# Kernel tuning notes

Hardware: AMD Instinct MI355X
Metric: run time of the kernel (lower is better)

## Reference

```python
import jax, jax.numpy as jnp
import numpy as np

N = 100000      # nodes
E = 1600000     # edges (avg degree 16)
D_IN = 128
CONV_SIZES = [64, 64]
FC_SIZES = [64, 32, 1]


def _glorot(key, shape):
    lim = np.sqrt(6.0 / (shape[0] + shape[1]))
    return jax.random.uniform(key, shape, jnp.float32, -lim, lim)


def setup_inputs() -> dict:
    key = jax.random.key(0)
    ks = jax.random.split(key, 2 + len(CONV_SIZES) + len(FC_SIZES))
    inp = {
        "x": jax.random.normal(ks[0], (N, D_IN), jnp.float32),
        "edge_index": jax.random.randint(ks[1], (2, E), 0, N, dtype=jnp.int64),
    }
    size = D_IN
    ki = 2
    for li, s in enumerate(CONV_SIZES):
        inp[f"cW{li}"] = _glorot(ks[ki], (size, s)); ki += 1
        inp[f"cb{li}"] = jnp.zeros((s,), jnp.float32)
        size = s
    for li, s in enumerate(FC_SIZES):
        inp[f"fW{li}"] = _glorot(ks[ki], (size, s)); ki += 1
        inp[f"fb{li}"] = jnp.zeros((s,), jnp.float32)
        size = s
    return inp


def gcn_conv(x, src, dst, W, b, n_nodes):
    """PyG GCNConv: symmetric normalization with added self-loops."""
    xl = x @ W  # [N, out]
    # degree including self-loop
    deg = jnp.zeros((n_nodes,), xl.dtype).at[dst].add(1.0) + 1.0
    dinv = jax.lax.rsqrt(deg)
    norm = dinv[src] * dinv[dst]                 # [E]
    msg = xl[src] * norm[:, None]                # gather + scale, [E, out]
    agg = jax.ops.segment_sum(msg, dst, num_segments=n_nodes)
    # self-loop contribution: norm = 1/deg
    return agg + xl * (1.0 / deg)[:, None] + b


def reference(x, edge_index, cW0, cb0, cW1, cb1, fW0, fb0, fW1, fb1, fW2, fb2):
    src, dst = edge_index[0], edge_index[1]
    h = jnp.tanh(gcn_conv(x, src, dst, cW0, cb0, N))
    h = jnp.tanh(gcn_conv(h, src, dst, cW1, cb1, N))
    h = jnp.tanh(h @ fW0 + fb0)
    h = jnp.tanh(h @ fW1 + fb1)
    return h @ fW2 + fb2  # [N, 1]
```

## Files before the change

### kernel.cpp

```cpp
#include <hip/hip_runtime.h>
#include <math.h>

#define N_NODES 100000
#define N_EDGES 1600000
#define NB     391
#define CHUNK  4096
#define NBLK_A 391

typedef unsigned short ushort_t;

__device__ inline unsigned short f2bf(float f) {
    unsigned u = __float_as_uint(f);
    unsigned r = (u + 0x7FFFu + ((u >> 16) & 1u)) >> 16;
    return (unsigned short)r;
}
__device__ inline void acc2(float& a0, float& a1, unsigned u) {
    a0 += __uint_as_float(u << 16);
    a1 += __uint_as_float(u & 0xFFFF0000u);
}


__global__ __launch_bounds__(256) void k_count(const int* __restrict__ dst,
                                               unsigned* __restrict__ cnt) {
    __shared__ unsigned h[NB];
    const int tid = threadIdx.x;
    const long e0 = (long)blockIdx.x * CHUNK;
    for (int i = tid; i < NB; i += 256) h[i] = 0u;
    __syncthreads();
    for (int i = tid; i < CHUNK; i += 256) {
        long e = e0 + i;
        if (e < N_EDGES) atomicAdd(&h[((unsigned)dst[e]) >> 8], 1u);
    }
    __syncthreads();
    for (int b = tid; b < NB; b += 256) cnt[b * NBLK_A + blockIdx.x] = h[b];
}

__global__ __launch_bounds__(512) void k_bucket_scan(unsigned* __restrict__ cnt,
                                                     unsigned* __restrict__ btot) {
    __shared__ unsigned s[512];
    const int tid = threadIdx.x;
    const int b = blockIdx.x;
    unsigned v = (tid < NBLK_A) ? cnt[b * NBLK_A + tid] : 0u;
    s[tid] = v;
    __syncthreads();
    for (int o = 1; o < 512; o <<= 1) {
        unsigned t = (tid >= o) ? s[tid - o] : 0u;
        __syncthreads();
        s[tid] += t;
        __syncthreads();
    }
    if (tid < NBLK_A) cnt[b * NBLK_A + tid] = s[tid] - v;
    if (tid == NBLK_A - 1) btot[b] = s[tid];
}

__global__ __launch_bounds__(512) void k_scan_bkt(const unsigned* __restrict__ btot,
                                                  unsigned* __restrict__ bktbase) {
    __shared__ unsigned s[512];
    const int tid = threadIdx.x;
    unsigned v = (tid < NB) ? btot[tid] : 0u;
    s[tid] = v;
    __syncthreads();
    for (int o = 1; o < 512; o <<= 1) {
        unsigned t = (tid >= o) ? s[tid - o] : 0u;
        __syncthreads();
        s[tid] += t;
        __syncthreads();
    }
    if (tid < NB) bktbase[tid] = s[tid] - v;
    if (tid == NB - 1) bktbase[NB] = s[tid];
}

__global__ __launch_bounds__(256) void k_bin(const int* __restrict__ src,
                                             const int* __restrict__ dst,
                                             const unsigned* __restrict__ cnt,
                                             const unsigned* __restrict__ bktbase,
                                             unsigned* __restrict__ binned) {
    __shared__ unsigned cntA[NB];
    __shared__ unsigned excl[NB];
    __shared__ unsigned gbase[NB];
    __shared__ unsigned scanbuf[512];
    __shared__ unsigned data[CHUNK];
    const int tid = threadIdx.x;
    const long e0 = (long)blockIdx.x * CHUNK;

    for (int i = tid; i < NB; i += 256) cntA[i] = 0u;
    __syncthreads();
    for (int i = tid; i < CHUNK; i += 256) {
        long e = e0 + i;
        if (e < N_EDGES) atomicAdd(&cntA[((unsigned)dst[e]) >> 8], 1u);
    }
    __syncthreads();
    scanbuf[tid] = (tid < NB) ? cntA[tid] : 0u;
    scanbuf[tid + 256] = (tid + 256 < NB) ? cntA[tid + 256] : 0u;
    __syncthreads();
    for (int o = 1; o < 512; o <<= 1) {
        unsigned v0 = (tid >= o) ? scanbuf[tid - o] : 0u;
        unsigned v1 = (tid + 256 >= o) ? scanbuf[tid + 256 - o] : 0u;
        __syncthreads();
        scanbuf[tid] += v0;
        scanbuf[tid + 256] += v1;
        __syncthreads();
    }
    for (int b = tid; b < NB; b += 256) {
        excl[b] = scanbuf[b] - cntA[b];
        gbase[b] = bktbase[b] + cnt[b * NBLK_A + blockIdx.x];
    }
    __syncthreads();
    for (int i = tid; i < NB; i += 256) cntA[i] = 0u;
    __syncthreads();
    for (int i = tid; i < CHUNK; i += 256) {
        long e = e0 + i;
        if (e < N_EDGES) {
            unsigned d = (unsigned)dst[e];
            unsigned b = d >> 8;
            unsigned slot = excl[b] + atomicAdd(&cntA[b], 1u);
            data[slot] = (((unsigned)src[e]) << 8) | (d & 255u);
        }
    }
    __syncthreads();
    const int w = tid >> 6, lane = tid & 63;
    for (int b = w; b < NB; b += 4) {
        unsigned c = cntA[b];
        unsigned sb = excl[b], gb = gbase[b];
        for (unsigned k = lane; k < c; k += 64)
            binned[gb + k] = data[sb + k];
    }
}

__global__ __launch_bounds__(256) void k_csr_fill2(const unsigned* __restrict__ binned,
                                                   const unsigned* __restrict__ bktbase,
                                                   unsigned* __restrict__ rowptr,
                                                   float* __restrict__ dinv,
                                                   int* __restrict__ ssrc) {
    __shared__ unsigned cnt[256];
    __shared__ unsigned s[256];
    __shared__ unsigned cur[256];
    const int b = blockIdx.x;
    const int tid = threadIdx.x;
    const int n0 = b * 256;
    const unsigned beg = bktbase[b], end = bktbase[b + 1];
    cnt[tid] = 0u;
    __syncthreads();
    for (unsigned i = beg + tid; i < end; i += 256)
        atomicAdd(&cnt[binned[i] & 255u], 1u);
    __syncthreads();
    const unsigned v = cnt[tid];
    s[tid] = v;
    __syncthreads();
    for (int o = 1; o < 256; o <<= 1) {
        unsigned t = (tid >= o) ? s[tid - o] : 0u;
        __syncthreads();
        s[tid] += t;
        __syncthreads();
    }
    const unsigned excl = s[tid] - v;
    const int node = n0 + tid;
    if (node < N_NODES) {
        rowptr[node] = beg + excl;
        dinv[node] = rsqrtf((float)(v + 1u));
        if (node == N_NODES - 1) rowptr[N_NODES] = end;
    }
    cur[tid] = beg + excl;
    __syncthreads();
    for (unsigned i = beg + tid; i < end; i += 256) {
        unsigned p = binned[i];
        unsigned pos = atomicAdd(&cur[p & 255u], 1u);
        ssrc[pos] = (int)(p >> 8);
    }
}


template<int K, int OUT>
__global__ __launch_bounds__(256) void k_gemm_bf(const float* __restrict__ A,
                                                 const float* __restrict__ W,
                                                 const float* __restrict__ dinv,
                                                 ushort_t* __restrict__ C) {
    constexpr int BR = 32;
    __shared__ float Wld[K * OUT];
    __shared__ float Ald[BR * K];
    const int tid = threadIdx.x;
    for (int i = tid; i < K * OUT; i += 256) Wld[i] = W[i];
    const long row0 = (long)blockIdx.x * BR;
    const float4* A4 = reinterpret_cast<const float4*>(A + row0 * K);
    float4* Ald4w = reinterpret_cast<float4*>(Ald);
    constexpr int NV = BR * K / 4;
    for (int i = tid; i < NV; i += 256) Ald4w[i] = A4[i];
    __syncthreads();

    constexpr int RG = 256 / OUT;
    constexpr int RPT = BR / RG;
    const int col = tid % OUT;
    const int rg = tid / OUT;
    const float4* Ald4 = reinterpret_cast<const float4*>(Ald);
    float acc[RPT];
#pragma unroll
    for (int j = 0; j < RPT; ++j) acc[j] = 0.f;
    for (int k4 = 0; k4 < K; k4 += 4) {
        const float w0 = Wld[(k4 + 0) * OUT + col];
        const float w1 = Wld[(k4 + 1) * OUT + col];
        const float w2 = Wld[(k4 + 2) * OUT + col];
        const float w3 = Wld[(k4 + 3) * OUT + col];
#pragma unroll
        for (int j = 0; j < RPT; ++j) {
            const float4 a = Ald4[((rg + j * RG) * K + k4) >> 2];
            acc[j] = fmaf(a.x, w0, fmaf(a.y, w1, fmaf(a.z, w2, fmaf(a.w, w3, acc[j]))));
        }
    }
#pragma unroll
    for (int j = 0; j < RPT; ++j) {
        const long r = row0 + rg + j * RG;
        C[r * OUT + col] = f2bf(acc[j] * dinv[r]);
    }
}

__global__ __launch_bounds__(256) void k_agg(const ushort_t* __restrict__ xlb,
                                             const float* __restrict__ dinv,
                                             const unsigned* __restrict__ rowptr,
                                             const int* __restrict__ ssrc,
                                             const float* __restrict__ bias,
                                             float* __restrict__ h) {
    const int node = blockIdx.x * 4 + (threadIdx.x >> 6);
    const int lane = threadIdx.x & 63;
    const int g = lane >> 3;
    const int l = lane & 7;
    const uint4* xb4 = reinterpret_cast<const uint4*>(xlb);

    const unsigned beg = rowptr[node], end = rowptr[node + 1];
    float a[8] = {0.f,0.f,0.f,0.f,0.f,0.f,0.f,0.f};
    float b[8] = {0.f,0.f,0.f,0.f,0.f,0.f,0.f,0.f};
    if (g == 0) {
        const uint4 v = xb4[(size_t)node * 8 + l];
        acc2(a[0], a[1], v.x); acc2(a[2], a[3], v.y);
        acc2(a[4], a[5], v.z); acc2(a[6], a[7], v.w);
    }
    unsigned j = beg + g;
    for (; j + 8 < end; j += 16) {
        const int s0 = ssrc[j];
        const int s1 = ssrc[j + 8];
        const uint4 v0 = xb4[(size_t)s0 * 8 + l];
        const uint4 v1 = xb4[(size_t)s1 * 8 + l];
        acc2(a[0], a[1], v0.x); acc2(a[2], a[3], v0.y);
        acc2(a[4], a[5], v0.z); acc2(a[6], a[7], v0.w);
        acc2(b[0], b[1], v1.x); acc2(b[2], b[3], v1.y);
        acc2(b[4], b[5], v1.z); acc2(b[6], b[7], v1.w);
    }
    if (j < end) {
        const uint4 v = xb4[(size_t)ssrc[j] * 8 + l];
        acc2(a[0], a[1], v.x); acc2(a[2], a[3], v.y);
        acc2(a[4], a[5], v.z); acc2(a[6], a[7], v.w);
    }
#pragma unroll
    for (int i = 0; i < 8; ++i) a[i] += b[i];
#pragma unroll
    for (int i = 0; i < 8; ++i) {
        a[i] += __shfl_xor(a[i], 8);
        a[i] += __shfl_xor(a[i], 16);
        a[i] += __shfl_xor(a[i], 32);
    }
    if (g == 0) {
        const float di = dinv[node];
        const float4 b0 = reinterpret_cast<const float4*>(bias)[l * 2];
        const float4 b1 = reinterpret_cast<const float4*>(bias)[l * 2 + 1];
        float4 r0, r1;
        r0.x = tanhf(fmaf(a[0], di, b0.x));
        r0.y = tanhf(fmaf(a[1], di, b0.y));
        r0.z = tanhf(fmaf(a[2], di, b0.z));
        r0.w = tanhf(fmaf(a[3], di, b0.w));
        r1.x = tanhf(fmaf(a[4], di, b1.x));
        r1.y = tanhf(fmaf(a[5], di, b1.y));
        r1.z = tanhf(fmaf(a[6], di, b1.z));
        r1.w = tanhf(fmaf(a[7], di, b1.w));
        float4* hp = reinterpret_cast<float4*>(h) + (size_t)node * 16 + l * 2;
        hp[0] = r0;
        hp[1] = r1;
    }
}

__global__ __launch_bounds__(256, 4) void k_fc(const float* __restrict__ h2,
                                               const float* __restrict__ fW0, const float* __restrict__ fb0,
                                               const float* __restrict__ fW1, const float* __restrict__ fb1,
                                               const float* __restrict__ fW2, const float* __restrict__ fb2,
                                               float* __restrict__ out) {
    constexpr int BR = 32;
    constexpr int LDH = 68;
    __shared__ float W0[64 * 64];
    __shared__ float W1[64 * 32];
    __shared__ float Hin[BR * LDH];
    __shared__ float Ht[BR * LDH];
    __shared__ float Hs[BR * 33];
    __shared__ float W2s[33];
    const int tid = threadIdx.x;
    {
        const float4* w04 = reinterpret_cast<const float4*>(fW0);
        float4* W04 = reinterpret_cast<float4*>(W0);
        for (int i = tid; i < 64 * 16; i += 256) W04[i] = w04[i];
        const float4* w14 = reinterpret_cast<const float4*>(fW1);
        float4* W14 = reinterpret_cast<float4*>(W1);
        for (int i = tid; i < 64 * 8; i += 256) W14[i] = w14[i];
        if (tid < 32) W2s[tid] = fW2[tid];
        if (tid == 32) W2s[32] = fb2[0];
    }
    const long row0 = (long)blockIdx.x * BR;
    {
        const float4* H4 = reinterpret_cast<const float4*>(h2 + row0 * 64);
        for (int i = tid; i < BR * 16; i += 256) {
            int r = i >> 4, q = i & 15;
            *reinterpret_cast<float4*>(&Hin[r * LDH + q * 4]) = H4[i];
        }
    }
    __syncthreads();

    {
        const int rp = tid >> 4;
        const int cq = tid & 15;
        const int r0 = rp * 2, r1 = r0 + 1;
        const float4 bias = reinterpret_cast<const float4*>(fb0)[cq];
        float4 acc0 = bias, acc1 = bias;
#pragma unroll 2
        for (int k4 = 0; k4 < 64; k4 += 4) {
            const float4 a0 = *reinterpret_cast<const float4*>(&Hin[r0 * LDH + k4]);
            const float4 a1 = *reinterpret_cast<const float4*>(&Hin[r1 * LDH + k4]);
            const float4 w0 = *reinterpret_cast<const float4*>(&W0[(k4 + 0) * 64 + cq * 4]);
            const float4 w1 = *reinterpret_cast<const float4*>(&W0[(k4 + 1) * 64 + cq * 4]);
            const float4 w2 = *reinterpret_cast<const float4*>(&W0[(k4 + 2) * 64 + cq * 4]);
            const float4 w3 = *reinterpret_cast<const float4*>(&W0[(k4 + 3) * 64 + cq * 4]);
            acc0.x = fmaf(a0.x, w0.x, fmaf(a0.y, w1.x, fmaf(a0.z, w2.x, fmaf(a0.w, w3.x, acc0.x))));
            acc0.y = fmaf(a0.x, w0.y, fmaf(a0.y, w1.y, fmaf(a0.z, w2.y, fmaf(a0.w, w3.y, acc0.y))));
            acc0.z = fmaf(a0.x, w0.z, fmaf(a0.y, w1.z, fmaf(a0.z, w2.z, fmaf(a0.w, w3.z, acc0.z))));
            acc0.w = fmaf(a0.x, w0.w, fmaf(a0.y, w1.w, fmaf(a0.z, w2.w, fmaf(a0.w, w3.w, acc0.w))));
            acc1.x = fmaf(a1.x, w0.x, fmaf(a1.y, w1.x, fmaf(a1.z, w2.x, fmaf(a1.w, w3.x, acc1.x))));
            acc1.y = fmaf(a1.x, w0.y, fmaf(a1.y, w1.y, fmaf(a1.z, w2.y, fmaf(a1.w, w3.y, acc1.y))));
            acc1.z = fmaf(a1.x, w0.z, fmaf(a1.y, w1.z, fmaf(a1.z, w2.z, fmaf(a1.w, w3.z, acc1.z))));
            acc1.w = fmaf(a1.x, w0.w, fmaf(a1.y, w1.w, fmaf(a1.z, w2.w, fmaf(a1.w, w3.w, acc1.w))));
        }
        float4 t0, t1;
        t0.x = tanhf(acc0.x); t0.y = tanhf(acc0.y); t0.z = tanhf(acc0.z); t0.w = tanhf(acc0.w);
        t1.x = tanhf(acc1.x); t1.y = tanhf(acc1.y); t1.z = tanhf(acc1.z); t1.w = tanhf(acc1.w);
        *reinterpret_cast<float4*>(&Ht[r0 * LDH + cq * 4]) = t0;
        *reinterpret_cast<float4*>(&Ht[r1 * LDH + cq * 4]) = t1;
    }
    __syncthreads();

    {
        const int r = tid >> 3;
        const int cq = tid & 7;
        const float4 bias = reinterpret_cast<const float4*>(fb1)[cq];
        float4 acc0 = bias;
#pragma unroll 2
        for (int k4 = 0; k4 < 64; k4 += 4) {
            const float4 a0 = *reinterpret_cast<const float4*>(&Ht[r * LDH + k4]);
            const float4 w0 = *reinterpret_cast<const float4*>(&W1[(k4 + 0) * 32 + cq * 4]);
            const float4 w1 = *reinterpret_cast<const float4*>(&W1[(k4 + 1) * 32 + cq * 4]);
            const float4 w2 = *reinterpret_cast<const float4*>(&W1[(k4 + 2) * 32 + cq * 4]);
            const float4 w3 = *reinterpret_cast<const float4*>(&W1[(k4 + 3) * 32 + cq * 4]);
            acc0.x = fmaf(a0.x, w0.x, fmaf(a0.y, w1.x, fmaf(a0.z, w2.x, fmaf(a0.w, w3.x, acc0.x))));
            acc0.y = fmaf(a0.x, w0.y, fmaf(a0.y, w1.y, fmaf(a0.z, w2.y, fmaf(a0.w, w3.y, acc0.y))));
            acc0.z = fmaf(a0.x, w0.z, fmaf(a0.y, w1.z, fmaf(a0.z, w2.z, fmaf(a0.w, w3.z, acc0.z))));
            acc0.w = fmaf(a0.x, w0.w, fmaf(a0.y, w1.w, fmaf(a0.z, w2.w, fmaf(a0.w, w3.w, acc0.w))));
        }
        Hs[r * 33 + cq * 4 + 0] = tanhf(acc0.x);
        Hs[r * 33 + cq * 4 + 1] = tanhf(acc0.y);
        Hs[r * 33 + cq * 4 + 2] = tanhf(acc0.z);
        Hs[r * 33 + cq * 4 + 3] = tanhf(acc0.w);
    }
    __syncthreads();

    if (tid < BR) {
        float a = W2s[32];
        for (int k = 0; k < 32; ++k) a = fmaf(Hs[tid * 33 + k], W2s[k], a);
        out[row0 + tid] = a;
    }
}


extern "C" void kernel_launch(void* const* d_in, const int* in_sizes, int n_in,
                              void* d_out, int out_size, void* d_ws, size_t ws_size,
                              hipStream_t stream) {
    const float* x    = (const float*)d_in[0];
    const int*   eidx = (const int*)d_in[1];
    const float* cW0  = (const float*)d_in[2];
    const float* cb0  = (const float*)d_in[3];
    const float* cW1  = (const float*)d_in[4];
    const float* cb1  = (const float*)d_in[5];
    const float* fW0  = (const float*)d_in[6];
    const float* fb0  = (const float*)d_in[7];
    const float* fW1  = (const float*)d_in[8];
    const float* fb1  = (const float*)d_in[9];
    const float* fW2  = (const float*)d_in[10];
    const float* fb2  = (const float*)d_in[11];
    float* out = (float*)d_out;

    const int* src = eidx;
    const int* dst = eidx + N_EDGES;

    char* ws = (char*)d_ws;
    unsigned* rowptr  = (unsigned*)(ws);
    float*    dinv    = (float*)   (ws + 400016);
    unsigned* cnt     = (unsigned*)(ws + 800016);
    unsigned* btot    = (unsigned*)(ws + 1411552);
    unsigned* bktbase = (unsigned*)(ws + 1413120);
    int*      ssrc    = (int*)     (ws + 1414688);
    ushort_t* xlb     = (ushort_t*)(ws + 7814688);
    unsigned* binned  = (unsigned*)(ws + 20614688);
    float*    bufB    = (float*)   (ws + 27014688);

    const int gRow = N_NODES / 32;
    const int gAgg = N_NODES / 4;

    k_count<<<NBLK_A, 256, 0, stream>>>(dst, cnt);
    k_bucket_scan<<<NB, 512, 0, stream>>>(cnt, btot);
    k_scan_bkt<<<1, 512, 0, stream>>>(btot, bktbase);
    k_bin<<<NBLK_A, 256, 0, stream>>>(src, dst, cnt, bktbase, binned);
    k_csr_fill2<<<NB, 256, 0, stream>>>(binned, bktbase, rowptr, dinv, ssrc);

    k_gemm_bf<128, 64><<<gRow, 256, 0, stream>>>(x, cW0, dinv, xlb);
    k_agg<<<gAgg, 256, 0, stream>>>(xlb, dinv, rowptr, ssrc, cb0, bufB);
    k_gemm_bf<64, 64><<<gRow, 256, 0, stream>>>(bufB, cW1, dinv, xlb);
    k_agg<<<gAgg, 256, 0, stream>>>(xlb, dinv, rowptr, ssrc, cb1, bufB);
    k_fc<<<gRow, 256, 0, stream>>>(bufB, fW0, fb0, fW1, fb1, fW2, fb2, out);
}
```

Baseline: 274.5 us.

## Rework aggregation lane mapping, use packed float2 adds and fast tanh

The aggregation kernel now gives each edge group 16 lanes that load 8-byte chunks instead of 8 lanes loading 16-byte chunks. After the shuffle reduction every lane produces one output feature, so the final tanh work is spread over all 64 lanes instead of 8. Accumulation uses 2-wide float vectors so the compiler can emit packed adds. tanhf in the aggregation and FC kernels is replaced by an exp/reciprocal approximation, which trades some accuracy and relies on large inputs saturating correctly.

```diff
diff --git a/kernel.cpp b/kernel.cpp
--- a/kernel.cpp
+++ b/kernel.cpp
@@ -8,15 +8,22 @@
 #define NBLK_A 391
 
 typedef unsigned short ushort_t;
+typedef __attribute__((ext_vector_type(2))) float f2v;
 
 __device__ inline unsigned short f2bf(float f) {
     unsigned u = __float_as_uint(f);
     unsigned r = (u + 0x7FFFu + ((u >> 16) & 1u)) >> 16;
     return (unsigned short)r;
 }
-__device__ inline void acc2(float& a0, float& a1, unsigned u) {
-    a0 += __uint_as_float(u << 16);
-    a1 += __uint_as_float(u & 0xFFFF0000u);
+__device__ inline void accp(f2v& a, unsigned u) {
+    f2v t;
+    t.x = __uint_as_float(u << 16);
+    t.y = __uint_as_float(u & 0xFFFF0000u);
+    a += t;
+}
+__device__ inline float fast_tanh(float x) {
+    float e = __expf(2.0f * x);
+    return fmaf(-2.0f, __builtin_amdgcn_rcpf(e + 1.0f), 1.0f);
 }
 
 
@@ -221,59 +228,42 @@
                                              float* __restrict__ h) {
     const int node = blockIdx.x * 4 + (threadIdx.x >> 6);
     const int lane = threadIdx.x & 63;
-    const int g = lane >> 3;
-    const int l = lane & 7;
-    const uint4* xb4 = reinterpret_cast<const uint4*>(xlb);
+    const int g = lane >> 4;
+    const int l = lane & 15;
+    const uint2* xb2 = reinterpret_cast<const uint2*>(xlb);
 
     const unsigned beg = rowptr[node], end = rowptr[node + 1];
-    float a[8] = {0.f,0.f,0.f,0.f,0.f,0.f,0.f,0.f};
-    float b[8] = {0.f,0.f,0.f,0.f,0.f,0.f,0.f,0.f};
+    f2v a0 = {0.f, 0.f}, a1 = {0.f, 0.f};
+    f2v b0 = {0.f, 0.f}, b1 = {0.f, 0.f};
     if (g == 0) {
-        const uint4 v = xb4[(size_t)node * 8 + l];
-        acc2(a[0], a[1], v.x); acc2(a[2], a[3], v.y);
-        acc2(a[4], a[5], v.z); acc2(a[6], a[7], v.w);
+        const uint2 v = xb2[(size_t)node * 16 + l];
+        accp(a0, v.x); accp(a1, v.y);
     }
     unsigned j = beg + g;
-    for (; j + 8 < end; j += 16) {
-        const int s0 = ssrc[j];
-        const int s1 = ssrc[j + 8];
-        const uint4 v0 = xb4[(size_t)s0 * 8 + l];
-        const uint4 v1 = xb4[(size_t)s1 * 8 + l];
-        acc2(a[0], a[1], v0.x); acc2(a[2], a[3], v0.y);
-        acc2(a[4], a[5], v0.z); acc2(a[6], a[7], v0.w);
-        acc2(b[0], b[1], v1.x); acc2(b[2], b[3], v1.y);
-        acc2(b[4], b[5], v1.z); acc2(b[6], b[7], v1.w);
+    for (; j + 4 < end; j += 8) {
+        const int s0i = ssrc[j];
+        const int s1i = ssrc[j + 4];
+        const uint2 v0 = xb2[(size_t)s0i * 16 + l];
+        const uint2 v1 = xb2[(size_t)s1i * 16 + l];
+        accp(a0, v0.x); accp(a1, v0.y);
+        accp(b0, v1.x); accp(b1, v1.y);
     }
     if (j < end) {
-        const uint4 v = xb4[(size_t)ssrc[j] * 8 + l];
-        acc2(a[0], a[1], v.x); acc2(a[2], a[3], v.y);
-        acc2(a[4], a[5], v.z); acc2(a[6], a[7], v.w);
-    }
-#pragma unroll
-    for (int i = 0; i < 8; ++i) a[i] += b[i];
-#pragma unroll
-    for (int i = 0; i < 8; ++i) {
-        a[i] += __shfl_xor(a[i], 8);
-        a[i] += __shfl_xor(a[i], 16);
-        a[i] += __shfl_xor(a[i], 32);
-    }
-    if (g == 0) {
-        const float di = dinv[node];
-        const float4 b0 = reinterpret_cast<const float4*>(bias)[l * 2];
-        const float4 b1 = reinterpret_cast<const float4*>(bias)[l * 2 + 1];
-        float4 r0, r1;
-        r0.x = tanhf(fmaf(a[0], di, b0.x));
-        r0.y = tanhf(fmaf(a[1], di, b0.y));
-        r0.z = tanhf(fmaf(a[2], di, b0.z));
-        r0.w = tanhf(fmaf(a[3], di, b0.w));
-        r1.x = tanhf(fmaf(a[4], di, b1.x));
-        r1.y = tanhf(fmaf(a[5], di, b1.y));
-        r1.z = tanhf(fmaf(a[6], di, b1.z));
-        r1.w = tanhf(fmaf(a[7], di, b1.w));
-        float4* hp = reinterpret_cast<float4*>(h) + (size_t)node * 16 + l * 2;
-        hp[0] = r0;
-        hp[1] = r1;
-    }
+        const uint2 v = xb2[(size_t)ssrc[j] * 16 + l];
+        accp(a0, v.x); accp(a1, v.y);
+    }
+    a0 += b0; a1 += b1;
+    float s0 = a0.x, s1 = a0.y, s2 = a1.x, s3 = a1.y;
+    s0 += __shfl_xor(s0, 16); s1 += __shfl_xor(s1, 16);
+    s2 += __shfl_xor(s2, 16); s3 += __shfl_xor(s3, 16);
+    s0 += __shfl_xor(s0, 32); s1 += __shfl_xor(s1, 32);
+    s2 += __shfl_xor(s2, 32); s3 += __shfl_xor(s3, 32);
+    const float t01 = (g & 1) ? s1 : s0;
+    const float t23 = (g & 1) ? s3 : s2;
+    const float v = (g & 2) ? t23 : t01;
+    const int f = l * 4 + g;
+    const float r = fast_tanh(fmaf(v, dinv[node], bias[f]));
+    h[(size_t)node * 64 + f] = r;
 }
 
 __global__ __launch_bounds__(256, 4) void k_fc(const float* __restrict__ h2,
@@ -334,8 +324,10 @@
             acc1.w = fmaf(a1.x, w0.w, fmaf(a1.y, w1.w, fmaf(a1.z, w2.w, fmaf(a1.w, w3.w, acc1.w))));
         }
         float4 t0, t1;
-        t0.x = tanhf(acc0.x); t0.y = tanhf(acc0.y); t0.z = tanhf(acc0.z); t0.w = tanhf(acc0.w);
-        t1.x = tanhf(acc1.x); t1.y = tanhf(acc1.y); t1.z = tanhf(acc1.z); t1.w = tanhf(acc1.w);
+        t0.x = fast_tanh(acc0.x); t0.y = fast_tanh(acc0.y);
+        t0.z = fast_tanh(acc0.z); t0.w = fast_tanh(acc0.w);
+        t1.x = fast_tanh(acc1.x); t1.y = fast_tanh(acc1.y);
+        t1.z = fast_tanh(acc1.z); t1.w = fast_tanh(acc1.w);
         *reinterpret_cast<float4*>(&Ht[r0 * LDH + cq * 4]) = t0;
         *reinterpret_cast<float4*>(&Ht[r1 * LDH + cq * 4]) = t1;
     }
@@ -358,10 +350,10 @@
             acc0.z = fmaf(a0.x, w0.z, fmaf(a0.y, w1.z, fmaf(a0.z, w2.z, fmaf(a0.w, w3.z, acc0.z))));
             acc0.w = fmaf(a0.x, w0.w, fmaf(a0.y, w1.w, fmaf(a0.z, w2.w, fmaf(a0.w, w3.w, acc0.w))));
         }
-        Hs[r * 33 + cq * 4 + 0] = tanhf(acc0.x);
-        Hs[r * 33 + cq * 4 + 1] = tanhf(acc0.y);
-        Hs[r * 33 + cq * 4 + 2] = tanhf(acc0.z);
-        Hs[r * 33 + cq * 4 + 3] = tanhf(acc0.w);
+        Hs[r * 33 + cq * 4 + 0] = fast_tanh(acc0.x);
+        Hs[r * 33 + cq * 4 + 1] = fast_tanh(acc0.y);
+        Hs[r * 33 + cq * 4 + 2] = fast_tanh(acc0.z);
+        Hs[r * 33 + cq * 4 + 3] = fast_tanh(acc0.w);
     }
     __syncthreads();
 
```

After: 270.3 us. No clear change (-1.5%).
